# Kernel tuning notes

Hardware: AMD Instinct MI355X
Metric: run time of the kernel (lower is better)

The kernel has to match this reference:

```python
import jax, jax.numpy as jnp
import numpy as np

NUM_USERS = 200000
NUM_ITEMS = 300000
EMBED_DIM = 64
N_LAYERS = 3
NNZ = 4000000
N_NODES = NUM_USERS + NUM_ITEMS


def setup_inputs() -> dict:
    key = jax.random.key(0)
    k1, k2, k3, k4, k5 = jax.random.split(key, 5)
    # Xavier-uniform-ish init scale for embeddings
    scale = np.sqrt(6.0 / (NUM_USERS + EMBED_DIM)).astype(np.float32)
    user_emb = jax.random.normal(k1, (NUM_USERS, EMBED_DIM), dtype=jnp.float32) * 0.01
    item_emb = jax.random.normal(k2, (NUM_ITEMS, EMBED_DIM), dtype=jnp.float32) * 0.01
    # COO representation of the symmetric-normalized adjacency (fixed structure)
    edge_row = jax.random.randint(k3, (NNZ,), 0, N_NODES, dtype=jnp.int32)
    edge_col = jax.random.randint(k4, (NNZ,), 0, N_NODES, dtype=jnp.int32)
    # normalized adjacency values ~ 1/sqrt(deg_i * deg_j), small positive
    edge_val = jax.random.uniform(k5, (NNZ,), dtype=jnp.float32) * 0.05
    return {
        "user_emb": user_emb,
        "item_emb": item_emb,
        "edge_row": edge_row,
        "edge_col": edge_col,
        "edge_val": edge_val,
    }


def reference(user_emb, item_emb, edge_row, edge_col, edge_val):
    # all_emb: [N_NODES, EMBED_DIM]
    all_emb = jnp.concatenate([user_emb, item_emb], axis=0)
    # Running accumulator for layer-mean (avoids stacking n_layers+1 copies)
    acc = all_emb
    for _ in range(N_LAYERS):
        # SpMM: out[i] = sum_{(i,j) in E} A[i,j] * all_emb[j]
        msgs = all_emb[edge_col] * edge_val[:, None]  # [NNZ, EMBED_DIM]
        all_emb = jax.ops.segment_sum(msgs, edge_row, num_segments=N_NODES)
        acc = acc + all_emb
    final = acc / jnp.float32(N_LAYERS + 1)
    users = final[:NUM_USERS]
    items = final[NUM_USERS:]
    return users, items
```

## Files before the change

kernel.cpp:

```cpp
#include <hip/hip_runtime.h>

#define NUSERS  200000
#define NITEMS  300000
#define NNODES  500000
#define DIM     64
#define NNZ_E   4000000
#define NBUCK   977
#define CAP     4864
#define VAL_Q   163820.0f
#define VAL_DQ  (1.0f / 163820.0f)
#define S0      2048.0f
#define INV_S1  (1.0f / 16384.0f)
#define INV_S2  (1.0f / 131072.0f)
#define UPSCALE 8.0f

typedef float f32x2 __attribute__((ext_vector_type(2)));
typedef float f32x4 __attribute__((ext_vector_type(4)));

__device__ inline unsigned enc_fp8x4(float x0, float x1, float x2, float x3) {
    int w = __builtin_amdgcn_cvt_pk_fp8_f32(x0, x1, 0, false);
    w = __builtin_amdgcn_cvt_pk_fp8_f32(x2, x3, w, true);
    return (unsigned)w;
}

#define GACC8(g, v)                                                      \
    do {                                                                 \
        f32x2 p0 = __builtin_amdgcn_cvt_pk_f32_fp8((int)(g).x, false);   \
        f32x2 p1 = __builtin_amdgcn_cvt_pk_f32_fp8((int)(g).x, true);    \
        f32x2 p2 = __builtin_amdgcn_cvt_pk_f32_fp8((int)(g).y, false);   \
        f32x2 p3 = __builtin_amdgcn_cvt_pk_f32_fp8((int)(g).y, true);    \
        a0 += p0.x * (v); a1 += p0.y * (v);                              \
        a2 += p1.x * (v); a3 += p1.y * (v);                              \
        a4 += p2.x * (v); a5 += p2.y * (v);                              \
        a6 += p3.x * (v); a7 += p3.y * (v);                              \
    } while (0)

__global__ void init_pack(const float4* __restrict__ user,
                          const float4* __restrict__ item,
                          uint4* __restrict__ tab) {
    int i = blockIdx.x * 256 + threadIdx.x;
    if (i >= NNODES * 4) return;
    int f4 = i * 4;
    const int nU4 = NUSERS * 16;
    const float4* src = (f4 < nU4) ? (user + f4) : (item + (f4 - nU4));
    float4 a = src[0], b = src[1], c = src[2], d = src[3];
    uint4 o;
    o.x = enc_fp8x4(a.x * S0, a.y * S0, a.z * S0, a.w * S0);
    o.y = enc_fp8x4(b.x * S0, b.y * S0, b.z * S0, b.w * S0);
    o.z = enc_fp8x4(c.x * S0, c.y * S0, c.z * S0, c.w * S0);
    o.w = enc_fp8x4(d.x * S0, d.y * S0, d.z * S0, d.w * S0);
    tab[i] = o;
}

__global__ __launch_bounds__(256) void partition_kernel(
        const int* __restrict__ erow, const int* __restrict__ ecol,
        const float* __restrict__ eval,
        int* __restrict__ bucketFill, uint2* __restrict__ part) {
    __shared__ int cnt[1024];
    __shared__ int off[1024];
    __shared__ int fill[1024];
    __shared__ int gbase[1024];
    __shared__ int tsum[256];
    __shared__ uint2 stage[4096];
    int tid = threadIdx.x;
    for (int b = tid; b < 1024; b += 256) { cnt[b] = 0; fill[b] = 0; }
    __syncthreads();

    int base = blockIdx.x * 4096;
    int n = NNZ_E - base; if (n > 4096) n = 4096;

    int myrow[16];
    unsigned mykey[16];
#pragma unroll
    for (int k = 0; k < 16; ++k) {
        int e = base + tid + k * 256;
        if (e < NNZ_E) {
            int r = erow[e];
            int c = ecol[e];
            float v = eval[e];
            int v13 = __float2int_rn(v * VAL_Q);
            if (v13 > 8191) v13 = 8191;
            if (v13 < 0) v13 = 0;
            myrow[k] = r;
            mykey[k] = (unsigned)c | ((unsigned)v13 << 19);
            atomicAdd(&cnt[r >> 9], 1);
        } else {
            myrow[k] = -1;
            mykey[k] = 0;
        }
    }
    __syncthreads();

    int t4 = tid * 4;
    int c0 = cnt[t4], c1 = cnt[t4 + 1], c2 = cnt[t4 + 2], c3 = cnt[t4 + 3];
    tsum[tid] = c0 + c1 + c2 + c3;
    __syncthreads();
    for (int d = 1; d < 256; d <<= 1) {
        int v = (tid >= d) ? tsum[tid - d] : 0;
        __syncthreads();
        tsum[tid] += v;
        __syncthreads();
    }
    int ex = (tid == 0) ? 0 : tsum[tid - 1];
    off[t4]     = ex;
    off[t4 + 1] = ex + c0;
    off[t4 + 2] = ex + c0 + c1;
    off[t4 + 3] = ex + c0 + c1 + c2;

    for (int b = tid; b < 1024; b += 256) {
        int c = cnt[b];
        gbase[b] = (c > 0) ? atomicAdd(&bucketFill[b], c) : 0;
    }
    __syncthreads();

#pragma unroll
    for (int k = 0; k < 16; ++k) {
        if (myrow[k] >= 0) {
            int b = myrow[k] >> 9;
            int slot = off[b] + atomicAdd(&fill[b], 1);
            stage[slot] = make_uint2(mykey[k], (unsigned)myrow[k]);
        }
    }
    __syncthreads();

    for (int s = tid; s < n; s += 256) {
        uint2 e = stage[s];
        int b = (int)(e.y >> 9);
        int idx = gbase[b] + (s - off[b]);
        if (idx < CAP) part[(size_t)b * CAP + idx] = e;
    }
}

__global__ void bucket_scan(const int* __restrict__ bucketFill,
                            int* __restrict__ bucketBase) {
    __shared__ int s[1024];
    int tid = threadIdx.x;
    int v = (tid < NBUCK) ? bucketFill[tid] : 0;
    s[tid] = v;
    __syncthreads();
    for (int d = 1; d < 1024; d <<= 1) {
        int t = (tid >= d) ? s[tid - d] : 0;
        __syncthreads();
        s[tid] += t;
        __syncthreads();
    }
    if (tid < NBUCK) bucketBase[tid] = s[tid] - v;
}

__global__ __launch_bounds__(256) void csr_build(
        const uint2* __restrict__ part, const int* __restrict__ bucketFill,
        const int* __restrict__ bucketBase,
        unsigned* __restrict__ csr, int* __restrict__ rowPtr) {
    __shared__ int rcnt[512], roff[512], rfill[512];
    __shared__ int tsum[256];
    int b = blockIdx.x;
    int tid = threadIdx.x;
    int lo = b * 512;
    int nE = bucketFill[b]; if (nE > CAP) nE = CAP;
    int base = bucketBase[b];
    const uint2* src = part + (size_t)b * CAP;

    for (int r = tid; r < 512; r += 256) { rcnt[r] = 0; rfill[r] = 0; }
    __syncthreads();
    for (int s = tid; s < nE; s += 256) {
        unsigned row = src[s].y;
        atomicAdd(&rcnt[row - lo], 1);
    }
    __syncthreads();
    int t2 = tid * 2;
    int c0 = rcnt[t2], c1 = rcnt[t2 + 1];
    tsum[tid] = c0 + c1;
    __syncthreads();
    for (int d = 1; d < 256; d <<= 1) {
        int v = (tid >= d) ? tsum[tid - d] : 0;
        __syncthreads();
        tsum[tid] += v;
        __syncthreads();
    }
    int ex = (tid == 0) ? 0 : tsum[tid - 1];
    roff[t2] = ex;
    roff[t2 + 1] = ex + c0;
    __syncthreads();
    for (int r = tid; r < 512; r += 256) {
        int row = lo + r;
        if (row < NNODES) rowPtr[row] = base + roff[r];
    }
    if (b == 0 && tid == 0) rowPtr[NNODES] = NNZ_E;
    for (int s = tid; s < nE; s += 256) {
        uint2 e = src[s];
        int r = (int)e.y - lo;
        int slot = base + roff[r] + atomicAdd(&rfill[r], 1);
        csr[slot] = e.x;
    }
}

__global__ __launch_bounds__(256) void spmv_kernel(
        const uint2* __restrict__ cur, uint2* __restrict__ next,
        const int* __restrict__ rowPtr, const unsigned* __restrict__ csr) {
    int t = blockIdx.x * 256 + threadIdx.x;
    int node = t >> 3;
    int lane = t & 7;
    if (node >= NNODES) return;
    int beg = rowPtr[node];
    int end = rowPtr[node + 1];
    float a0 = 0, a1 = 0, a2 = 0, a3 = 0, a4 = 0, a5 = 0, a6 = 0, a7 = 0;
    int j = beg;
    for (; j + 4 <= end; j += 4) {
        unsigned e0 = csr[j], e1 = csr[j + 1], e2 = csr[j + 2], e3 = csr[j + 3];
        uint2 g0 = cur[(e0 & 0x7FFFFu) * 8 + lane];
        uint2 g1 = cur[(e1 & 0x7FFFFu) * 8 + lane];
        uint2 g2 = cur[(e2 & 0x7FFFFu) * 8 + lane];
        uint2 g3 = cur[(e3 & 0x7FFFFu) * 8 + lane];
        float v0 = (float)(e0 >> 19) * VAL_DQ;
        float v1 = (float)(e1 >> 19) * VAL_DQ;
        float v2 = (float)(e2 >> 19) * VAL_DQ;
        float v3 = (float)(e3 >> 19) * VAL_DQ;
        GACC8(g0, v0);
        GACC8(g1, v1);
        GACC8(g2, v2);
        GACC8(g3, v3);
    }
    for (; j < end; ++j) {
        unsigned e = csr[j];
        float v = (float)(e >> 19) * VAL_DQ;
        uint2 g = cur[(e & 0x7FFFFu) * 8 + lane];
        GACC8(g, v);
    }
    uint2 o;
    o.x = enc_fp8x4(a0 * UPSCALE, a1 * UPSCALE, a2 * UPSCALE, a3 * UPSCALE);
    o.y = enc_fp8x4(a4 * UPSCALE, a5 * UPSCALE, a6 * UPSCALE, a7 * UPSCALE);
    next[node * 8 + lane] = o;
}

__global__ __launch_bounds__(256) void spmv_final_kernel(
        const uint2* __restrict__ c8,
        const uint2* __restrict__ b8,
        const float* __restrict__ user, const float* __restrict__ item,
        float* __restrict__ out,
        const int* __restrict__ rowPtr, const unsigned* __restrict__ csr) {
    int t = blockIdx.x * 256 + threadIdx.x;
    int node = t >> 3;
    int lane = t & 7;
    if (node >= NNODES) return;
    int beg = rowPtr[node];
    int end = rowPtr[node + 1];
    float a0 = 0, a1 = 0, a2 = 0, a3 = 0, a4 = 0, a5 = 0, a6 = 0, a7 = 0;
    int j = beg;
    for (; j + 4 <= end; j += 4) {
        unsigned e0 = csr[j], e1 = csr[j + 1], e2 = csr[j + 2], e3 = csr[j + 3];
        uint2 g0 = c8[(e0 & 0x7FFFFu) * 8 + lane];
        uint2 g1 = c8[(e1 & 0x7FFFFu) * 8 + lane];
        uint2 g2 = c8[(e2 & 0x7FFFFu) * 8 + lane];
        uint2 g3 = c8[(e3 & 0x7FFFFu) * 8 + lane];
        float v0 = (float)(e0 >> 19) * VAL_DQ;
        float v1 = (float)(e1 >> 19) * VAL_DQ;
        float v2 = (float)(e2 >> 19) * VAL_DQ;
        float v3 = (float)(e3 >> 19) * VAL_DQ;
        GACC8(g0, v0);
        GACC8(g1, v1);
        GACC8(g2, v2);
        GACC8(g3, v3);
    }
    for (; j < end; ++j) {
        unsigned e = csr[j];
        float v = (float)(e >> 19) * VAL_DQ;
        uint2 g = c8[(e & 0x7FFFFu) * 8 + lane];
        GACC8(g, v);
    }

    int idx = node * 8 + lane;
    uint2 ub = b8[idx];
    uint2 uc = c8[idx];
    f32x2 b01 = __builtin_amdgcn_cvt_pk_f32_fp8((int)ub.x, false);
    f32x2 b23 = __builtin_amdgcn_cvt_pk_f32_fp8((int)ub.x, true);
    f32x2 b45 = __builtin_amdgcn_cvt_pk_f32_fp8((int)ub.y, false);
    f32x2 b67 = __builtin_amdgcn_cvt_pk_f32_fp8((int)ub.y, true);
    f32x2 c01 = __builtin_amdgcn_cvt_pk_f32_fp8((int)uc.x, false);
    f32x2 c23 = __builtin_amdgcn_cvt_pk_f32_fp8((int)uc.x, true);
    f32x2 c45 = __builtin_amdgcn_cvt_pk_f32_fp8((int)uc.y, false);
    f32x2 c67 = __builtin_amdgcn_cvt_pk_f32_fp8((int)uc.y, true);

    const float* ebase = (node < NUSERS)
        ? (user + (size_t)node * DIM)
        : (item + (size_t)(node - NUSERS) * DIM);
    f32x4 e01 = *(const f32x4*)(ebase + lane * 8);
    f32x4 e23 = *(const f32x4*)(ebase + lane * 8 + 4);

    f32x4 o01, o23;
    o01.x = (e01.x + b01.x * INV_S1 + (c01.x + a0) * INV_S2) * 0.25f;
    o01.y = (e01.y + b01.y * INV_S1 + (c01.y + a1) * INV_S2) * 0.25f;
    o01.z = (e01.z + b23.x * INV_S1 + (c23.x + a2) * INV_S2) * 0.25f;
    o01.w = (e01.w + b23.y * INV_S1 + (c23.y + a3) * INV_S2) * 0.25f;
    o23.x = (e23.x + b45.x * INV_S1 + (c45.x + a4) * INV_S2) * 0.25f;
    o23.y = (e23.y + b45.y * INV_S1 + (c45.y + a5) * INV_S2) * 0.25f;
    o23.z = (e23.z + b67.x * INV_S1 + (c67.x + a6) * INV_S2) * 0.25f;
    o23.w = (e23.w + b67.y * INV_S1 + (c67.y + a7) * INV_S2) * 0.25f;
    f32x4* dst = (f32x4*)(out + (size_t)node * DIM + lane * 8);
    __builtin_nontemporal_store(o01, dst);
    __builtin_nontemporal_store(o23, dst + 1);
}

extern "C" void kernel_launch(void* const* d_in, const int* in_sizes, int n_in,
                              void* d_out, int out_size, void* d_ws, size_t ws_size,
                              hipStream_t stream) {
    const float* user = (const float*)d_in[0];
    const float* item = (const float*)d_in[1];
    const int*   erow = (const int*)d_in[2];
    const int*   ecol = (const int*)d_in[3];
    const float* eval = (const float*)d_in[4];
    float* out = (float*)d_out;

    const size_t tabBytes = (size_t)NNODES * DIM;
    char* ws = (char*)d_ws;
    size_t ofs = 0;
    auto alloc = [&](size_t bytes) {
        void* p = ws + ofs;
        ofs = (ofs + bytes + 255) & ~(size_t)255;
        return p;
    };
    uint2* A8 = (uint2*)alloc(tabBytes);
    uint2* B8 = (uint2*)alloc(tabBytes);
    uint2* C8 = (uint2*)alloc(tabBytes);
    uint2* part       = (uint2*)alloc((size_t)NBUCK * CAP * sizeof(uint2));
    unsigned* csr     = (unsigned*)alloc((size_t)NNZ_E * sizeof(unsigned));
    int* rowPtr       = (int*)alloc((NNODES + 1) * sizeof(int));
    int* bucketFill   = (int*)alloc(1024 * sizeof(int));
    int* bucketBase   = (int*)alloc(1024 * sizeof(int));

    init_pack<<<(NNODES * 4 + 255) / 256, 256, 0, stream>>>(
        (const float4*)user, (const float4*)item, (uint4*)A8);

    (void)hipMemsetAsync(bucketFill, 0, 1024 * sizeof(int), stream);
    const int partBlocks = (NNZ_E + 4095) / 4096;
    partition_kernel<<<partBlocks, 256, 0, stream>>>(erow, ecol, eval,
                                                     bucketFill, part);
    bucket_scan<<<1, 1024, 0, stream>>>(bucketFill, bucketBase);
    csr_build<<<NBUCK, 256, 0, stream>>>(part, bucketFill, bucketBase,
                                         csr, rowPtr);

    const int spmvBlocks = (NNODES * 8) / 256;
    spmv_kernel<<<spmvBlocks, 256, 0, stream>>>(A8, B8, rowPtr, csr);
    spmv_kernel<<<spmvBlocks, 256, 0, stream>>>(B8, C8, rowPtr, csr);
    spmv_final_kernel<<<spmvBlocks, 256, 0, stream>>>(C8, B8, user, item,
                                                      out, rowPtr, csr);
}
```

Before: 386.7 us.

## Drop bucket scan kernel; allocate CSR ranges atomically and pack row count into rowPtr

```diff
diff --git a/kernel.cpp b/kernel.cpp
--- a/kernel.cpp
+++ b/kernel.cpp
@@ -131,41 +131,31 @@
     }
 }
 
-__global__ void bucket_scan(const int* __restrict__ bucketFill,
-                            int* __restrict__ bucketBase) {
-    __shared__ int s[1024];
-    int tid = threadIdx.x;
-    int v = (tid < NBUCK) ? bucketFill[tid] : 0;
-    s[tid] = v;
-    __syncthreads();
-    for (int d = 1; d < 1024; d <<= 1) {
-        int t = (tid >= d) ? s[tid - d] : 0;
-        __syncthreads();
-        s[tid] += t;
-        __syncthreads();
-    }
-    if (tid < NBUCK) bucketBase[tid] = s[tid] - v;
-}
-
 __global__ __launch_bounds__(256) void csr_build(
         const uint2* __restrict__ part, const int* __restrict__ bucketFill,
-        const int* __restrict__ bucketBase,
-        unsigned* __restrict__ csr, int* __restrict__ rowPtr) {
+        int* __restrict__ csrCounter,
+        unsigned* __restrict__ csr, unsigned* __restrict__ rowPtr) {
+    __shared__ unsigned  lkey[CAP];
+    __shared__ unsigned short lrlo[CAP];
     __shared__ int rcnt[512], roff[512], rfill[512];
     __shared__ int tsum[256];
+    __shared__ int sbase;
     int b = blockIdx.x;
     int tid = threadIdx.x;
     int lo = b * 512;
     int nE = bucketFill[b]; if (nE > CAP) nE = CAP;
-    int base = bucketBase[b];
     const uint2* src = part + (size_t)b * CAP;
 
     for (int r = tid; r < 512; r += 256) { rcnt[r] = 0; rfill[r] = 0; }
     __syncthreads();
     for (int s = tid; s < nE; s += 256) {
-        unsigned row = src[s].y;
-        atomicAdd(&rcnt[row - lo], 1);
-    }
+        uint2 e = src[s];
+        int rl = (int)e.y - lo;
+        lkey[s] = e.x;
+        lrlo[s] = (unsigned short)rl;
+        atomicAdd(&rcnt[rl], 1);
+    }
+    if (tid == 0) sbase = atomicAdd(csrCounter, nE);
     __syncthreads();
     int t2 = tid * 2;
     int c0 = rcnt[t2], c1 = rcnt[t2 + 1];
@@ -181,28 +171,29 @@
     roff[t2] = ex;
     roff[t2 + 1] = ex + c0;
     __syncthreads();
+    int base = sbase;
     for (int r = tid; r < 512; r += 256) {
         int row = lo + r;
-        if (row < NNODES) rowPtr[row] = base + roff[r];
-    }
-    if (b == 0 && tid == 0) rowPtr[NNODES] = NNZ_E;
+        if (row < NNODES)
+            rowPtr[row] = (unsigned)(base + roff[r]) | ((unsigned)rcnt[r] << 22);
+    }
     for (int s = tid; s < nE; s += 256) {
-        uint2 e = src[s];
-        int r = (int)e.y - lo;
-        int slot = base + roff[r] + atomicAdd(&rfill[r], 1);
-        csr[slot] = e.x;
+        int rl = lrlo[s];
+        int slot = base + roff[rl] + atomicAdd(&rfill[rl], 1);
+        csr[slot] = lkey[s];
     }
 }
 
 __global__ __launch_bounds__(256) void spmv_kernel(
         const uint2* __restrict__ cur, uint2* __restrict__ next,
-        const int* __restrict__ rowPtr, const unsigned* __restrict__ csr) {
+        const unsigned* __restrict__ rowPtr, const unsigned* __restrict__ csr) {
     int t = blockIdx.x * 256 + threadIdx.x;
     int node = t >> 3;
     int lane = t & 7;
     if (node >= NNODES) return;
-    int beg = rowPtr[node];
-    int end = rowPtr[node + 1];
+    unsigned u = rowPtr[node];
+    int beg = (int)(u & 0x3FFFFFu);
+    int end = beg + (int)(u >> 22);
     float a0 = 0, a1 = 0, a2 = 0, a3 = 0, a4 = 0, a5 = 0, a6 = 0, a7 = 0;
     int j = beg;
     for (; j + 4 <= end; j += 4) {
@@ -237,13 +228,14 @@
         const uint2* __restrict__ b8,
         const float* __restrict__ user, const float* __restrict__ item,
         float* __restrict__ out,
-        const int* __restrict__ rowPtr, const unsigned* __restrict__ csr) {
+        const unsigned* __restrict__ rowPtr, const unsigned* __restrict__ csr) {
     int t = blockIdx.x * 256 + threadIdx.x;
     int node = t >> 3;
     int lane = t & 7;
     if (node >= NNODES) return;
-    int beg = rowPtr[node];
-    int end = rowPtr[node + 1];
+    unsigned u = rowPtr[node];
+    int beg = (int)(u & 0x3FFFFFu);
+    int end = beg + (int)(u >> 22);
     float a0 = 0, a1 = 0, a2 = 0, a3 = 0, a4 = 0, a5 = 0, a6 = 0, a7 = 0;
     int j = beg;
     for (; j + 4 <= end; j += 4) {
@@ -321,21 +313,19 @@
     uint2* A8 = (uint2*)alloc(tabBytes);
     uint2* B8 = (uint2*)alloc(tabBytes);
     uint2* C8 = (uint2*)alloc(tabBytes);
-    uint2* part       = (uint2*)alloc((size_t)NBUCK * CAP * sizeof(uint2));
-    unsigned* csr     = (unsigned*)alloc((size_t)NNZ_E * sizeof(unsigned));
-    int* rowPtr       = (int*)alloc((NNODES + 1) * sizeof(int));
-    int* bucketFill   = (int*)alloc(1024 * sizeof(int));
-    int* bucketBase   = (int*)alloc(1024 * sizeof(int));
+    uint2* part     = (uint2*)alloc((size_t)NBUCK * CAP * sizeof(uint2));
+    unsigned* csr   = (unsigned*)alloc((size_t)NNZ_E * sizeof(unsigned));
+    unsigned* rowPtr = (unsigned*)alloc(NNODES * sizeof(unsigned));
+    int* ints       = (int*)alloc(1025 * sizeof(int));
 
     init_pack<<<(NNODES * 4 + 255) / 256, 256, 0, stream>>>(
         (const float4*)user, (const float4*)item, (uint4*)A8);
 
-    (void)hipMemsetAsync(bucketFill, 0, 1024 * sizeof(int), stream);
+    (void)hipMemsetAsync(ints, 0, 1025 * sizeof(int), stream);
     const int partBlocks = (NNZ_E + 4095) / 4096;
     partition_kernel<<<partBlocks, 256, 0, stream>>>(erow, ecol, eval,
-                                                     bucketFill, part);
-    bucket_scan<<<1, 1024, 0, stream>>>(bucketFill, bucketBase);
-    csr_build<<<NBUCK, 256, 0, stream>>>(part, bucketFill, bucketBase,
+                                                     ints, part);
+    csr_build<<<NBUCK, 256, 0, stream>>>(part, ints, ints + 1024,
                                          csr, rowPtr);
 
     const int spmvBlocks = (NNODES * 8) / 256;
```

New measurement: 392.0 us. About the same (+1.4%).
